# Performance work log

Measured on AMD Instinct MI355X. Metric: run time of the kernel, lower is better.

## Reference

```python
import jax, jax.numpy as jnp
import numpy as np

N = 100_000      # nodes
E = 3_200_000    # edges (avg degree 32)
D_IN = 128
D_H = 128
EPS = 1e-12      # F.normalize eps


def setup_inputs() -> dict:
    key = jax.random.key(0)
    k1, k2, k3 = jax.random.split(key, 3)
    X = jax.random.normal(k1, (N, D_IN), dtype=jnp.float32)
    edge_index = jax.random.randint(k2, (2, E), 0, N, dtype=jnp.int32)
    # GCNConv linear weight (stored as [in, out] for X @ W) and bias
    W = jax.random.normal(k3, (D_IN, D_H), dtype=jnp.float32) / np.sqrt(D_IN)
    b = jnp.zeros((D_H,), dtype=jnp.float32)
    # MessageNorm learnable scale, init 1.0
    scale = jnp.ones((1,), dtype=jnp.float32)
    return {"X": X, "edge_index": edge_index, "W": W, "b": b, "scale": scale}


def reference(X, edge_index, W, b, scale):
    n = X.shape[0]
    loop = jnp.arange(n, dtype=edge_index.dtype)
    src = jnp.concatenate([edge_index[0], loop])  # add self loops
    tgt = jnp.concatenate([edge_index[1], loop])
    # symmetric GCN normalization: D^{-1/2} (A+I) D^{-1/2}
    deg = jax.ops.segment_sum(jnp.ones_like(src, X.dtype), tgt, num_segments=n)
    dinv = jnp.where(deg > 0, jax.lax.rsqrt(deg), 0.0)
    norm = dinv[src] * dinv[tgt]  # [E+N]
    XW = X @ W  # [N, D_H]
    msg = jax.ops.segment_sum(norm[:, None] * XW[src], tgt, num_segments=n) + b
    # MessageNorm(learn_scale=True): l2-normalize msg, rescale by ||x||_2 * scale
    msg_n = msg / jnp.maximum(jnp.linalg.norm(msg, axis=-1, keepdims=True), EPS)
    x_norm = jnp.linalg.norm(X, axis=-1, keepdims=True)
    return jax.nn.gelu(msg_n * x_norm * scale, approximate=False)
```

## Files before the change

### kernel.cpp

```cpp
#include <hip/hip_runtime.h>
#include <math.h>

#define D 128
#define NB 391
#define BSH 8
#define BMASK 255
#define CAP 9216
#define EPB 4096
#define LDA 136

typedef unsigned short ushort_t;
typedef unsigned int uint_t;
typedef __attribute__((ext_vector_type(8))) short bfrag;
typedef __attribute__((ext_vector_type(4))) float ffrag;

__device__ inline ushort_t f2bf(float f) {
    uint_t u = __float_as_uint(f);
    uint_t r = (u + 0x7FFFu + ((u >> 16) & 1u)) >> 16;
    return (ushort_t)r;
}

__global__ __launch_bounds__(256) void k_bin(const int* __restrict__ src,
                                             const int* __restrict__ tgt, int e,
                                             int* __restrict__ bucket_cur,
                                             uint_t* __restrict__ binned,
                                             const float* __restrict__ W,
                                             ushort_t* __restrict__ Wt) {
    __shared__ uint_t sval[EPB];
    __shared__ ushort_t sbkt[EPB];
    __shared__ int lcnt[NB];
    __shared__ int lbeg[NB];
    __shared__ int gbase[NB];
    __shared__ int pscan[256];
    int tid = threadIdx.x;

    if (blockIdx.x < 16) {
        int nrow = blockIdx.x * 8 + (tid >> 5);
        int k0 = (tid & 31) * 4;
        ushort4 o;
        o.x = f2bf(W[(size_t)(k0 + 0) * D + nrow]);
        o.y = f2bf(W[(size_t)(k0 + 1) * D + nrow]);
        o.z = f2bf(W[(size_t)(k0 + 2) * D + nrow]);
        o.w = f2bf(W[(size_t)(k0 + 3) * D + nrow]);
        *(ushort4*)&Wt[(size_t)nrow * D + k0] = o;
    }

    int base = blockIdx.x * EPB;
    for (int i = tid; i < NB; i += 256) lcnt[i] = 0;
    __syncthreads();

    int myb[16];
    uint_t myval[16];
#pragma unroll
    for (int k = 0; k < 16; ++k) {
        int i = base + k * 256 + tid;
        if (i < e) {
            int t = tgt[i];
            int s = src[i];
            myb[k] = t >> BSH;
            myval[k] = ((uint_t)s << BSH) | (uint_t)(t & BMASK);
            atomicAdd(&lcnt[myb[k]], 1);
        } else {
            myb[k] = -1;
        }
    }
    __syncthreads();

    int c0 = (2 * tid < NB) ? lcnt[2 * tid] : 0;
    int c1 = (2 * tid + 1 < NB) ? lcnt[2 * tid + 1] : 0;
    int x = c0 + c1;
    pscan[tid] = x;
    __syncthreads();
    for (int off = 1; off < 256; off <<= 1) {
        int y = (tid >= off) ? pscan[tid - off] : 0;
        __syncthreads();
        x += y;
        pscan[tid] = x;
        __syncthreads();
    }
    int pb = x - (c0 + c1);
    if (2 * tid < NB) lbeg[2 * tid] = pb;
    if (2 * tid + 1 < NB) lbeg[2 * tid + 1] = pb + c0;
    __syncthreads();

    for (int i = tid; i < NB; i += 256) {
        int c = lcnt[i];
        gbase[i] = (c > 0) ? atomicAdd(&bucket_cur[i], c) : 0;
        lcnt[i] = lbeg[i];
    }
    __syncthreads();

#pragma unroll
    for (int k = 0; k < 16; ++k) {
        if (myb[k] >= 0) {
            int r = atomicAdd(&lcnt[myb[k]], 1);
            sval[r] = myval[k];
            sbkt[r] = (ushort_t)myb[k];
        }
    }
    __syncthreads();

    int nb = min(e - base, EPB);
    for (int i = tid; i < nb; i += 256) {
        int b = sbkt[i];
        int slot = gbase[b] + (i - lbeg[b]);
        if (slot < CAP) binned[(size_t)b * CAP + slot] = sval[i];
    }
}

__global__ __launch_bounds__(256) void k_mid(uint_t* __restrict__ binned,
                                             const int* __restrict__ bucket_cur,
                                             int* __restrict__ rowinfo,
                                             float* __restrict__ dinv,
                                             const float* __restrict__ X,
                                             const ushort_t* __restrict__ Wt,
                                             ushort_t* __restrict__ Y,
                                             float* __restrict__ xnorm, int n) {
    __shared__ __align__(16) char smem[52224];
    int tid = threadIdx.x;

    if (blockIdx.x < NB) {
        uint_t* sout = (uint_t*)smem;
        int* scnt  = (int*)(smem + CAP * 4);
        int* sincl = scnt + 256;
        int* sofs  = sincl + 256;
        int b = blockIdx.x;

        int nb = min(bucket_cur[b], CAP);
        uint_t* bin = binned + (size_t)b * CAP;

        scnt[tid] = 0;
        __syncthreads();
        for (int i = tid; i < nb; i += 256)
            atomicAdd(&scnt[bin[i] & BMASK], 1);
        __syncthreads();
        int x = scnt[tid];
        sincl[tid] = x;
        __syncthreads();
        for (int off = 1; off < 256; off <<= 1) {
            int y = (tid >= off) ? sincl[tid - off] : 0;
            __syncthreads();
            x += y;
            sincl[tid] = x;
            __syncthreads();
        }
        sofs[tid] = x - scnt[tid];
        int t = (b << BSH) + tid;
        if (t < n) {
            rowinfo[t] = ((x - scnt[tid]) << 16) | x;
            dinv[t] = rsqrtf((float)scnt[tid] + 1.0f);
        }
        __syncthreads();
        for (int i = tid; i < nb; i += 256) {
            uint_t w = bin[i];
            int r = atomicAdd(&sofs[w & BMASK], 1);
            sout[r] = w >> BSH;
        }
        __syncthreads();
        for (int i = tid; i < nb; i += 256)
            bin[i] = sout[i];
    } else {
        ushort_t* As = (ushort_t*)smem;
        ushort_t* Bs = (ushort_t*)(smem + 17408);
        int row0 = (blockIdx.x - NB) * 64;

        for (int i = tid; i < 128 * 16; i += 256) {
            int nr = i >> 4, c = (i & 15) << 3;
            *(uint4*)&Bs[nr * LDA + c] = *(const uint4*)&Wt[(size_t)nr * D + c];
        }

        const float4* X4 = (const float4*)X;
#pragma unroll
        for (int i2 = 0; i2 < 8; ++i2) {
            int item = i2 * 256 + tid;
            int r = item >> 5, c4 = item & 31;
            int gr = row0 + r;
            float4 vv = (gr < n) ? X4[(size_t)gr * 32 + c4] : make_float4(0.f, 0.f, 0.f, 0.f);
            ushort4 bv;
            bv.x = f2bf(vv.x); bv.y = f2bf(vv.y); bv.z = f2bf(vv.z); bv.w = f2bf(vv.w);
            *(ushort4*)&As[r * LDA + c4 * 4] = bv;
            float s = vv.x * vv.x + vv.y * vv.y + vv.z * vv.z + vv.w * vv.w;
            s += __shfl_xor(s, 1);
            s += __shfl_xor(s, 2);
            s += __shfl_xor(s, 4);
            s += __shfl_xor(s, 8);
            s += __shfl_xor(s, 16);
            if ((tid & 31) == 0 && gr < n) xnorm[gr] = sqrtf(s);
        }
        __syncthreads();

        int w = tid >> 6;
        int lane = tid & 63;
        int q = lane >> 4;
        int mi = lane & 15;

        bfrag xf[4];
#pragma unroll
        for (int kt = 0; kt < 4; ++kt)
            xf[kt] = *(const bfrag*)&As[(w * 16 + mi) * LDA + kt * 32 + q * 8];

        ffrag acc[8];
#pragma unroll
        for (int nt = 0; nt < 8; ++nt) acc[nt] = (ffrag){0.f, 0.f, 0.f, 0.f};

#pragma unroll
        for (int nt = 0; nt < 8; ++nt) {
#pragma unroll
            for (int kt = 0; kt < 4; ++kt) {
                bfrag wf = *(const bfrag*)&Bs[(nt * 16 + mi) * LDA + kt * 32 + q * 8];
                acc[nt] = __builtin_amdgcn_mfma_f32_16x16x32_bf16(wf, xf[kt], acc[nt], 0, 0, 0);
            }
        }

        __syncthreads();
#pragma unroll
        for (int nt = 0; nt < 8; ++nt) {
            ushort4 o;
            o.x = f2bf(acc[nt][0]);
            o.y = f2bf(acc[nt][1]);
            o.z = f2bf(acc[nt][2]);
            o.w = f2bf(acc[nt][3]);
            *(ushort4*)&As[(w * 16 + mi) * LDA + nt * 16 + q * 4] = o;
        }
        __syncthreads();

        int row = tid >> 2, seg = tid & 3;
        int grow = row0 + row;
        if (grow < n) {
#pragma unroll
            for (int k2 = 0; k2 < 4; ++k2) {
                uint4 vv = *(const uint4*)&As[row * LDA + seg * 32 + k2 * 8];
                *(uint4*)&Y[(size_t)grow * D + seg * 32 + k2 * 8] = vv;
            }
        }
    }
}

__global__ __launch_bounds__(256) void k_agg(const ushort_t* __restrict__ Y,
                                             const float* __restrict__ xnorm,
                                             const float* __restrict__ dinv,
                                             const int* __restrict__ rowinfo,
                                             const uint_t* __restrict__ binned,
                                             const float* __restrict__ bias,
                                             const float* __restrict__ scale,
                                             float* __restrict__ out, int n) {
    int t = (blockIdx.x * 256 + threadIdx.x) >> 6;
    int lane = threadIdx.x & 63;
    if (t >= n) return;

    const char* Yb = (const char*)Y;
    uint_t lo4 = (uint_t)lane * 4;
    float dt = dinv[t];

    uint_t p = *(const uint_t*)(Yb + (((uint_t)t << 8) + lo4));
    float a0 = dt * __uint_as_float(p << 16);
    float a1 = dt * __uint_as_float(p & 0xFFFF0000u);

    int ri = rowinfo[t];
    int slice = (t >> BSH) * CAP;
    int beg = slice + (ri >> 16);
    int end = slice + (ri & 0xFFFF);
    for (int base = beg; base < end; base += 64) {
        int m = min(end - base, 64);
        uint_t cv = binned[base + min(lane, m - 1)];
        int k = 0;
        for (; k + 16 <= m; k += 16) {
            uint_t qv[16];
            float dv[16];
#pragma unroll
            for (int j = 0; j < 16; ++j) {
                int s = __builtin_amdgcn_readlane((int)cv, k + j);
                dv[j] = dinv[s];
                qv[j] = *(const uint_t*)(Yb + ((size_t)(uint_t)s << 8) + lo4);
            }
#pragma unroll
            for (int j = 0; j < 16; ++j) {
                a0 = fmaf(dv[j], __uint_as_float(qv[j] << 16), a0);
                a1 = fmaf(dv[j], __uint_as_float(qv[j] & 0xFFFF0000u), a1);
            }
        }
        for (; k + 4 <= m; k += 4) {
            uint_t qv[4];
            float dv[4];
#pragma unroll
            for (int j = 0; j < 4; ++j) {
                int s = __builtin_amdgcn_readlane((int)cv, k + j);
                dv[j] = dinv[s];
                qv[j] = *(const uint_t*)(Yb + ((size_t)(uint_t)s << 8) + lo4);
            }
#pragma unroll
            for (int j = 0; j < 4; ++j) {
                a0 = fmaf(dv[j], __uint_as_float(qv[j] << 16), a0);
                a1 = fmaf(dv[j], __uint_as_float(qv[j] & 0xFFFF0000u), a1);
            }
        }
        for (; k < m; ++k) {
            int s = __builtin_amdgcn_readlane((int)cv, k);
            float dvs = dinv[s];
            uint_t q = *(const uint_t*)(Yb + ((size_t)(uint_t)s << 8) + lo4);
            a0 = fmaf(dvs, __uint_as_float(q << 16), a0);
            a1 = fmaf(dvs, __uint_as_float(q & 0xFFFF0000u), a1);
        }
    }

    float m0 = fmaf(dt, a0, bias[lane * 2]);
    float m1 = fmaf(dt, a1, bias[lane * 2 + 1]);

    float m2 = m0 * m0 + m1 * m1;
#pragma unroll
    for (int m = 32; m >= 1; m >>= 1) m2 += __shfl_xor(m2, m);

    float denom = fmaxf(sqrtf(m2), 1e-12f);
    float fac = xnorm[t] * scale[0] / denom;
    float g0 = m0 * fac;
    float g1 = m1 * fac;
    float2 o;
    o.x = 0.5f * g0 * (1.0f + erff(g0 * 0.70710678118654752440f));
    o.y = 0.5f * g1 * (1.0f + erff(g1 * 0.70710678118654752440f));
    *(float2*)&out[(size_t)t * D + lane * 2] = o;
}


extern "C" void kernel_launch(void* const* d_in, const int* in_sizes, int n_in,
                              void* d_out, int out_size, void* d_ws, size_t ws_size,
                              hipStream_t stream) {
    const float* X     = (const float*)d_in[0];
    const int*   ei    = (const int*)d_in[1];
    const float* W     = (const float*)d_in[2];
    const float* bias  = (const float*)d_in[3];
    const float* scale = (const float*)d_in[4];
    float* out = (float*)d_out;

    int n = in_sizes[0] / D;
    int e = in_sizes[1] / 2;
    const int* src = ei;
    const int* tgt = ei + e;

    char* ws = (char*)d_ws;
    ushort_t* Y = (ushort_t*)ws;   ws += (size_t)n * D * sizeof(ushort_t);
    uint_t* binned = (uint_t*)ws;  ws += (size_t)NB * CAP * sizeof(uint_t);
    float* dinv = (float*)ws;      ws += (size_t)n * sizeof(float);
    float* xnorm = (float*)ws;     ws += (size_t)n * sizeof(float);
    int* rowinfo = (int*)ws;       ws += (size_t)n * sizeof(int);
    int* bucket_cur = (int*)ws;    ws += NB * sizeof(int);
    ushort_t* Wt = (ushort_t*)ws;

    int ngemm = (n + 63) / 64;

    hipMemsetAsync(bucket_cur, 0, NB * sizeof(int), stream);
    k_bin<<<(e + EPB - 1) / EPB, 256, 0, stream>>>(src, tgt, e, bucket_cur, binned, W, Wt);
    k_mid<<<NB + ngemm, 256, 0, stream>>>(binned, bucket_cur, rowinfo, dinv, X, Wt, Y, xnorm, n);
    k_agg<<<(n + 3) / 4, 256, 0, stream>>>(Y, xnorm, dinv, rowinfo, binned, bias, scale, out, n);
}
```

Measured before the change: 288.4 us.

## Fuse bin, sort, GEMM and aggregation into one cooperative persistent kernel

Merges the memset and the three launches into a single cooperative kernel that uses grid.sync between phases, with a fallback to separate launches if the cooperative launch fails. The aim is to cut launch gaps and raise occupancy through smaller shared memory. Bucket size drops to 128 targets with half-sized chunks, so binning writes directly through per-thread ranks instead of staging in shared memory. The scans now use wave shuffles, and the GEMM reads W fragments from global memory instead of staging them in LDS. The costs are grid-wide barrier overhead, persistent-loop imbalance, and uncoalesced scattered binned writes.

```diff
diff --git a/kernel.cpp b/kernel.cpp
--- a/kernel.cpp
+++ b/kernel.cpp
@@ -1,13 +1,18 @@
 #include <hip/hip_runtime.h>
+#include <hip/hip_cooperative_groups.h>
 #include <math.h>
 
+namespace cg = cooperative_groups;
+
 #define D 128
-#define NB 391
-#define BSH 8
-#define BMASK 255
-#define CAP 9216
-#define EPB 4096
+#define BSH 7
+#define BMASK 127
+#define NT 128
+#define NB 782
+#define CAP 4608
+#define EPB 2048
 #define LDA 136
+#define SMEM_BYTES 20480
 
 typedef unsigned short ushort_t;
 typedef unsigned int uint_t;
@@ -20,22 +25,17 @@
     return (ushort_t)r;
 }
 
-__global__ __launch_bounds__(256) void k_bin(const int* __restrict__ src,
-                                             const int* __restrict__ tgt, int e,
-                                             int* __restrict__ bucket_cur,
-                                             uint_t* __restrict__ binned,
-                                             const float* __restrict__ W,
-                                             ushort_t* __restrict__ Wt) {
-    __shared__ uint_t sval[EPB];
-    __shared__ ushort_t sbkt[EPB];
-    __shared__ int lcnt[NB];
-    __shared__ int lbeg[NB];
-    __shared__ int gbase[NB];
-    __shared__ int pscan[256];
+__device__ void dev_bin(int v, int e, char* smem, const int* __restrict__ src,
+                        const int* __restrict__ tgt, int* __restrict__ bucket_cur,
+                        uint_t* __restrict__ binned, const float* __restrict__ W,
+                        ushort_t* __restrict__ Wt) {
+    int* lcnt = (int*)smem;
+    int* lbase = lcnt + NB;
     int tid = threadIdx.x;
-
-    if (blockIdx.x < 16) {
-        int nrow = blockIdx.x * 8 + (tid >> 5);
+    __syncthreads();
+
+    if (v < 16) {
+        int nrow = v * 8 + (tid >> 5);
         int k0 = (tid & 31) * 4;
         ushort4 o;
         o.x = f2bf(W[(size_t)(k0 + 0) * D + nrow]);
@@ -45,209 +45,173 @@
         *(ushort4*)&Wt[(size_t)nrow * D + k0] = o;
     }
 
-    int base = blockIdx.x * EPB;
+    int base = v * EPB;
     for (int i = tid; i < NB; i += 256) lcnt[i] = 0;
     __syncthreads();
 
-    int myb[16];
-    uint_t myval[16];
-#pragma unroll
-    for (int k = 0; k < 16; ++k) {
+    int myb[8], myrank[8];
+    uint_t myval[8];
+#pragma unroll
+    for (int k = 0; k < 8; ++k) {
         int i = base + k * 256 + tid;
         if (i < e) {
             int t = tgt[i];
             int s = src[i];
             myb[k] = t >> BSH;
             myval[k] = ((uint_t)s << BSH) | (uint_t)(t & BMASK);
-            atomicAdd(&lcnt[myb[k]], 1);
+            myrank[k] = atomicAdd(&lcnt[myb[k]], 1);
         } else {
             myb[k] = -1;
         }
     }
     __syncthreads();
-
-    int c0 = (2 * tid < NB) ? lcnt[2 * tid] : 0;
-    int c1 = (2 * tid + 1 < NB) ? lcnt[2 * tid + 1] : 0;
-    int x = c0 + c1;
-    pscan[tid] = x;
-    __syncthreads();
-    for (int off = 1; off < 256; off <<= 1) {
-        int y = (tid >= off) ? pscan[tid - off] : 0;
-        __syncthreads();
-        x += y;
-        pscan[tid] = x;
-        __syncthreads();
-    }
-    int pb = x - (c0 + c1);
-    if (2 * tid < NB) lbeg[2 * tid] = pb;
-    if (2 * tid + 1 < NB) lbeg[2 * tid + 1] = pb + c0;
-    __syncthreads();
-
     for (int i = tid; i < NB; i += 256) {
         int c = lcnt[i];
-        gbase[i] = (c > 0) ? atomicAdd(&bucket_cur[i], c) : 0;
-        lcnt[i] = lbeg[i];
-    }
-    __syncthreads();
-
-#pragma unroll
-    for (int k = 0; k < 16; ++k) {
+        lbase[i] = (c > 0) ? atomicAdd(&bucket_cur[i], c) : 0;
+    }
+    __syncthreads();
+#pragma unroll
+    for (int k = 0; k < 8; ++k) {
         if (myb[k] >= 0) {
-            int r = atomicAdd(&lcnt[myb[k]], 1);
-            sval[r] = myval[k];
-            sbkt[r] = (ushort_t)myb[k];
-        }
-    }
-    __syncthreads();
-
-    int nb = min(e - base, EPB);
-    for (int i = tid; i < nb; i += 256) {
-        int b = sbkt[i];
-        int slot = gbase[b] + (i - lbeg[b]);
-        if (slot < CAP) binned[(size_t)b * CAP + slot] = sval[i];
-    }
-}
-
-__global__ __launch_bounds__(256) void k_mid(uint_t* __restrict__ binned,
-                                             const int* __restrict__ bucket_cur,
-                                             int* __restrict__ rowinfo,
-                                             float* __restrict__ dinv,
-                                             const float* __restrict__ X,
-                                             const ushort_t* __restrict__ Wt,
-                                             ushort_t* __restrict__ Y,
-                                             float* __restrict__ xnorm, int n) {
-    __shared__ __align__(16) char smem[52224];
+            int slot = lbase[myb[k]] + myrank[k];
+            if (slot < CAP) binned[(size_t)myb[k] * CAP + slot] = myval[k];
+        }
+    }
+}
+
+__device__ void dev_sort(int b, int n, char* smem, uint_t* __restrict__ binned,
+                         const int* __restrict__ bucket_cur, int* __restrict__ rowinfo,
+                         float* __restrict__ dinv) {
+    uint_t* sout = (uint_t*)smem;
+    int* scnt = (int*)(smem + CAP * 4);
+    int* sbeg = scnt + NT;
+    int* sofs = sbeg + NT;
     int tid = threadIdx.x;
-
-    if (blockIdx.x < NB) {
-        uint_t* sout = (uint_t*)smem;
-        int* scnt  = (int*)(smem + CAP * 4);
-        int* sincl = scnt + 256;
-        int* sofs  = sincl + 256;
-        int b = blockIdx.x;
-
-        int nb = min(bucket_cur[b], CAP);
-        uint_t* bin = binned + (size_t)b * CAP;
-
-        scnt[tid] = 0;
-        __syncthreads();
-        for (int i = tid; i < nb; i += 256)
-            atomicAdd(&scnt[bin[i] & BMASK], 1);
-        __syncthreads();
-        int x = scnt[tid];
-        sincl[tid] = x;
-        __syncthreads();
-        for (int off = 1; off < 256; off <<= 1) {
-            int y = (tid >= off) ? sincl[tid - off] : 0;
-            __syncthreads();
-            x += y;
-            sincl[tid] = x;
-            __syncthreads();
-        }
-        sofs[tid] = x - scnt[tid];
+    int lane = tid & 63;
+    __syncthreads();
+
+    int nb = min(bucket_cur[b], CAP);
+    uint_t* bin = binned + (size_t)b * CAP;
+
+    if (tid < NT) scnt[tid] = 0;
+    __syncthreads();
+    for (int i = tid; i < nb; i += 256)
+        atomicAdd(&scnt[bin[i] & BMASK], 1);
+    __syncthreads();
+    if (tid < 64) {
+        int c0 = scnt[lane];
+        int c1 = scnt[lane + 64];
+        int x0 = c0, x1 = c1;
+#pragma unroll
+        for (int off = 1; off < 64; off <<= 1) {
+            int y0 = __shfl_up(x0, off);
+            int y1 = __shfl_up(x1, off);
+            if (lane >= off) { x0 += y0; x1 += y1; }
+        }
+        int tot0 = __shfl(x0, 63);
+        x1 += tot0;
+        sbeg[lane] = x0 - c0;      sofs[lane] = x0 - c0;
+        sbeg[lane + 64] = x1 - c1; sofs[lane + 64] = x1 - c1;
+    }
+    __syncthreads();
+    if (tid < NT) {
         int t = (b << BSH) + tid;
         if (t < n) {
-            rowinfo[t] = ((x - scnt[tid]) << 16) | x;
+            int beg = sbeg[tid];
+            rowinfo[t] = (beg << 16) | (beg + scnt[tid]);
             dinv[t] = rsqrtf((float)scnt[tid] + 1.0f);
         }
-        __syncthreads();
-        for (int i = tid; i < nb; i += 256) {
-            uint_t w = bin[i];
-            int r = atomicAdd(&sofs[w & BMASK], 1);
-            sout[r] = w >> BSH;
-        }
-        __syncthreads();
-        for (int i = tid; i < nb; i += 256)
-            bin[i] = sout[i];
-    } else {
-        ushort_t* As = (ushort_t*)smem;
-        ushort_t* Bs = (ushort_t*)(smem + 17408);
-        int row0 = (blockIdx.x - NB) * 64;
-
-        for (int i = tid; i < 128 * 16; i += 256) {
-            int nr = i >> 4, c = (i & 15) << 3;
-            *(uint4*)&Bs[nr * LDA + c] = *(const uint4*)&Wt[(size_t)nr * D + c];
-        }
-
-        const float4* X4 = (const float4*)X;
-#pragma unroll
-        for (int i2 = 0; i2 < 8; ++i2) {
-            int item = i2 * 256 + tid;
-            int r = item >> 5, c4 = item & 31;
-            int gr = row0 + r;
-            float4 vv = (gr < n) ? X4[(size_t)gr * 32 + c4] : make_float4(0.f, 0.f, 0.f, 0.f);
-            ushort4 bv;
-            bv.x = f2bf(vv.x); bv.y = f2bf(vv.y); bv.z = f2bf(vv.z); bv.w = f2bf(vv.w);
-            *(ushort4*)&As[r * LDA + c4 * 4] = bv;
-            float s = vv.x * vv.x + vv.y * vv.y + vv.z * vv.z + vv.w * vv.w;
-            s += __shfl_xor(s, 1);
-            s += __shfl_xor(s, 2);
-            s += __shfl_xor(s, 4);
-            s += __shfl_xor(s, 8);
-            s += __shfl_xor(s, 16);
-            if ((tid & 31) == 0 && gr < n) xnorm[gr] = sqrtf(s);
-        }
-        __syncthreads();
-
-        int w = tid >> 6;
-        int lane = tid & 63;
-        int q = lane >> 4;
-        int mi = lane & 15;
-
-        bfrag xf[4];
-#pragma unroll
-        for (int kt = 0; kt < 4; ++kt)
-            xf[kt] = *(const bfrag*)&As[(w * 16 + mi) * LDA + kt * 32 + q * 8];
-
-        ffrag acc[8];
-#pragma unroll
-        for (int nt = 0; nt < 8; ++nt) acc[nt] = (ffrag){0.f, 0.f, 0.f, 0.f};
-
-#pragma unroll
-        for (int nt = 0; nt < 8; ++nt) {
-#pragma unroll
-            for (int kt = 0; kt < 4; ++kt) {
-                bfrag wf = *(const bfrag*)&Bs[(nt * 16 + mi) * LDA + kt * 32 + q * 8];
-                acc[nt] = __builtin_amdgcn_mfma_f32_16x16x32_bf16(wf, xf[kt], acc[nt], 0, 0, 0);
-            }
-        }
-
-        __syncthreads();
-#pragma unroll
-        for (int nt = 0; nt < 8; ++nt) {
-            ushort4 o;
-            o.x = f2bf(acc[nt][0]);
-            o.y = f2bf(acc[nt][1]);
-            o.z = f2bf(acc[nt][2]);
-            o.w = f2bf(acc[nt][3]);
-            *(ushort4*)&As[(w * 16 + mi) * LDA + nt * 16 + q * 4] = o;
-        }
-        __syncthreads();
-
-        int row = tid >> 2, seg = tid & 3;
-        int grow = row0 + row;
-        if (grow < n) {
-#pragma unroll
-            for (int k2 = 0; k2 < 4; ++k2) {
-                uint4 vv = *(const uint4*)&As[row * LDA + seg * 32 + k2 * 8];
-                *(uint4*)&Y[(size_t)grow * D + seg * 32 + k2 * 8] = vv;
-            }
-        }
-    }
-}
-
-__global__ __launch_bounds__(256) void k_agg(const ushort_t* __restrict__ Y,
-                                             const float* __restrict__ xnorm,
-                                             const float* __restrict__ dinv,
-                                             const int* __restrict__ rowinfo,
-                                             const uint_t* __restrict__ binned,
-                                             const float* __restrict__ bias,
-                                             const float* __restrict__ scale,
-                                             float* __restrict__ out, int n) {
-    int t = (blockIdx.x * 256 + threadIdx.x) >> 6;
+    }
+    __syncthreads();
+    for (int i = tid; i < nb; i += 256) {
+        uint_t w = bin[i];
+        int r = atomicAdd(&sofs[w & BMASK], 1);
+        sout[r] = w >> BSH;
+    }
+    __syncthreads();
+    for (int i = tid; i < nb; i += 256)
+        bin[i] = sout[i];
+}
+
+__device__ void dev_gemm(int u, int n, char* smem, const float* __restrict__ X,
+                         const ushort_t* __restrict__ Wt, ushort_t* __restrict__ Y,
+                         float* __restrict__ xnorm) {
+    ushort_t* As = (ushort_t*)smem;
+    int tid = threadIdx.x;
+    int row0 = u * 64;
+    __syncthreads();
+
+    const float4* X4 = (const float4*)X;
+#pragma unroll
+    for (int i2 = 0; i2 < 8; ++i2) {
+        int item = i2 * 256 + tid;
+        int r = item >> 5, c4 = item & 31;
+        int gr = row0 + r;
+        float4 v = (gr < n) ? X4[(size_t)gr * 32 + c4] : make_float4(0.f, 0.f, 0.f, 0.f);
+        ushort4 bv;
+        bv.x = f2bf(v.x); bv.y = f2bf(v.y); bv.z = f2bf(v.z); bv.w = f2bf(v.w);
+        *(ushort4*)&As[r * LDA + c4 * 4] = bv;
+        float s = v.x * v.x + v.y * v.y + v.z * v.z + v.w * v.w;
+        s += __shfl_xor(s, 1);
+        s += __shfl_xor(s, 2);
+        s += __shfl_xor(s, 4);
+        s += __shfl_xor(s, 8);
+        s += __shfl_xor(s, 16);
+        if ((tid & 31) == 0 && gr < n) xnorm[gr] = sqrtf(s);
+    }
+    __syncthreads();
+
+    int w = tid >> 6;
+    int lane = tid & 63;
+    int q = lane >> 4;
+    int mi = lane & 15;
+
+    bfrag xf[4];
+#pragma unroll
+    for (int kt = 0; kt < 4; ++kt)
+        xf[kt] = *(const bfrag*)&As[(w * 16 + mi) * LDA + kt * 32 + q * 8];
+
+    ffrag acc[8];
+#pragma unroll
+    for (int nt = 0; nt < 8; ++nt) acc[nt] = (ffrag){0.f, 0.f, 0.f, 0.f};
+
+#pragma unroll
+    for (int nt = 0; nt < 8; ++nt) {
+#pragma unroll
+        for (int kt = 0; kt < 4; ++kt) {
+            bfrag wf = *(const bfrag*)&Wt[(size_t)(nt * 16 + mi) * D + kt * 32 + q * 8];
+            acc[nt] = __builtin_amdgcn_mfma_f32_16x16x32_bf16(wf, xf[kt], acc[nt], 0, 0, 0);
+        }
+    }
+
+    __syncthreads();
+#pragma unroll
+    for (int nt = 0; nt < 8; ++nt) {
+        ushort4 o;
+        o.x = f2bf(acc[nt][0]);
+        o.y = f2bf(acc[nt][1]);
+        o.z = f2bf(acc[nt][2]);
+        o.w = f2bf(acc[nt][3]);
+        *(ushort4*)&As[(w * 16 + mi) * LDA + nt * 16 + q * 4] = o;
+    }
+    __syncthreads();
+
+    int row = tid >> 2, seg = tid & 3;
+    int grow = row0 + row;
+    if (grow < n) {
+#pragma unroll
+        for (int k2 = 0; k2 < 4; ++k2) {
+            uint4 vv = *(const uint4*)&As[row * LDA + seg * 32 + k2 * 8];
+            *(uint4*)&Y[(size_t)grow * D + seg * 32 + k2 * 8] = vv;
+        }
+    }
+}
+
+__device__ void dev_agg(int t, const ushort_t* __restrict__ Y, const float* __restrict__ xnorm,
+                        const float* __restrict__ dinv, const int* __restrict__ rowinfo,
+                        const uint_t* __restrict__ binned, float b0, float b1, float sc,
+                        float* __restrict__ out) {
     int lane = threadIdx.x & 63;
-    if (t >= n) return;
-
     const char* Yb = (const char*)Y;
     uint_t lo4 = (uint_t)lane * 4;
     float dt = dinv[t];
@@ -303,21 +267,83 @@
         }
     }
 
-    float m0 = fmaf(dt, a0, bias[lane * 2]);
-    float m1 = fmaf(dt, a1, bias[lane * 2 + 1]);
-
+    float m0 = fmaf(dt, a0, b0);
+    float m1 = fmaf(dt, a1, b1);
     float m2 = m0 * m0 + m1 * m1;
 #pragma unroll
-    for (int m = 32; m >= 1; m >>= 1) m2 += __shfl_xor(m2, m);
-
+    for (int mm = 32; mm >= 1; mm >>= 1) m2 += __shfl_xor(m2, mm);
     float denom = fmaxf(sqrtf(m2), 1e-12f);
-    float fac = xnorm[t] * scale[0] / denom;
+    float fac = xnorm[t] * sc / denom;
     float g0 = m0 * fac;
     float g1 = m1 * fac;
     float2 o;
     o.x = 0.5f * g0 * (1.0f + erff(g0 * 0.70710678118654752440f));
     o.y = 0.5f * g1 * (1.0f + erff(g1 * 0.70710678118654752440f));
     *(float2*)&out[(size_t)t * D + lane * 2] = o;
+}
+
+__global__ __launch_bounds__(256, 6) void k_all(const int* src, const int* tgt, int e,
+                                                int* bucket_cur, uint_t* binned,
+                                                const float* W, ushort_t* Wt,
+                                                const float* X, ushort_t* Y, float* xnorm,
+                                                float* dinv, int* rowinfo,
+                                                const float* bias, const float* scale,
+                                                float* out, int n, int nchunk, int ngemm) {
+    cg::grid_group grid = cg::this_grid();
+    __shared__ __align__(16) char smem[SMEM_BYTES];
+    int nblk = gridDim.x;
+    int tid = threadIdx.x;
+
+    for (int i = blockIdx.x * 256 + tid; i < NB; i += nblk * 256) bucket_cur[i] = 0;
+    grid.sync();
+
+    for (int v = blockIdx.x; v < nchunk; v += nblk)
+        dev_bin(v, e, smem, src, tgt, bucket_cur, binned, W, Wt);
+    grid.sync();
+
+    int ntot = NB + ngemm;
+    for (int v = blockIdx.x; v < ntot; v += nblk) {
+        if (v < NB) dev_sort(v, n, smem, binned, bucket_cur, rowinfo, dinv);
+        else        dev_gemm(v - NB, n, smem, X, Wt, Y, xnorm);
+    }
+    grid.sync();
+
+    int lane = tid & 63;
+    float b0 = bias[lane * 2];
+    float b1 = bias[lane * 2 + 1];
+    float sc = scale[0];
+    int wid = blockIdx.x * 4 + (tid >> 6);
+    int nw = nblk * 4;
+    for (int t = wid; t < n; t += nw)
+        dev_agg(t, Y, xnorm, dinv, rowinfo, binned, b0, b1, sc, out);
+}
+
+__global__ __launch_bounds__(256) void k_bin_s(const int* src, const int* tgt, int e,
+                                               int* bucket_cur, uint_t* binned,
+                                               const float* W, ushort_t* Wt) {
+    __shared__ __align__(16) char smem[8192];
+    dev_bin(blockIdx.x, e, smem, src, tgt, bucket_cur, binned, W, Wt);
+}
+
+__global__ __launch_bounds__(256) void k_mid_s(uint_t* binned, const int* bucket_cur,
+                                               int* rowinfo, float* dinv, const float* X,
+                                               const ushort_t* Wt, ushort_t* Y,
+                                               float* xnorm, int n) {
+    __shared__ __align__(16) char smem[SMEM_BYTES];
+    int v = blockIdx.x;
+    if (v < NB) dev_sort(v, n, smem, binned, bucket_cur, rowinfo, dinv);
+    else        dev_gemm(v - NB, n, smem, X, Wt, Y, xnorm);
+}
+
+__global__ __launch_bounds__(256) void k_agg_s(const ushort_t* Y, const float* xnorm,
+                                               const float* dinv, const int* rowinfo,
+                                               const uint_t* binned, const float* bias,
+                                               const float* scale, float* out, int n) {
+    int t = (blockIdx.x * 256 + threadIdx.x) >> 6;
+    if (t >= n) return;
+    int lane = threadIdx.x & 63;
+    dev_agg(t, Y, xnorm, dinv, rowinfo, binned, bias[lane * 2], bias[lane * 2 + 1],
+            scale[0], out);
 }
 
 
@@ -345,10 +371,36 @@
     int* bucket_cur = (int*)ws;    ws += NB * sizeof(int);
     ushort_t* Wt = (ushort_t*)ws;
 
+    int nchunk = (e + EPB - 1) / EPB;
     int ngemm = (n + 63) / 64;
 
-    hipMemsetAsync(bucket_cur, 0, NB * sizeof(int), stream);
-    k_bin<<<(e + EPB - 1) / EPB, 256, 0, stream>>>(src, tgt, e, bucket_cur, binned, W, Wt);
-    k_mid<<<NB + ngemm, 256, 0, stream>>>(binned, bucket_cur, rowinfo, dinv, X, Wt, Y, xnorm, n);
-    k_agg<<<(n + 3) / 4, 256, 0, stream>>>(Y, xnorm, dinv, rowinfo, binned, bias, scale, out, n);
-}
+    static int coopGrid = -2;
+    if (coopGrid == -2) {
+        int occ = 0;
+        hipError_t oe = hipOccupancyMaxActiveBlocksPerMultiprocessor(&occ, k_all, 256, 0);
+        coopGrid = (oe == hipSuccess && occ >= 1) ? ((occ < 8 ? occ : 8) * 256) : -1;
+    }
+
+    bool done = false;
+    if (coopGrid > 0) {
+        const int* srcp = src; const int* tgtp = tgt;
+        int ev = e, nv = n, ncv = nchunk, ngv = ngemm;
+        int* bcur = bucket_cur; uint_t* binp = binned;
+        const float* Wp = W; ushort_t* Wtp = Wt;
+        const float* Xp = X; ushort_t* Yp = Y;
+        float* xnp = xnorm; float* dvp = dinv; int* rip = rowinfo;
+        const float* bp = bias; const float* scp = scale; float* op = out;
+        void* args[] = {&srcp, &tgtp, &ev, &bcur, &binp, &Wp, &Wtp, &Xp, &Yp,
+                        &xnp, &dvp, &rip, &bp, &scp, &op, &nv, &ncv, &ngv};
+        hipError_t err = hipLaunchCooperativeKernel((const void*)k_all, dim3(coopGrid),
+                                                    dim3(256), args, 0, stream);
+        if (err == hipSuccess) done = true;
+        else coopGrid = -1;
+    }
+    if (!done) {
+        hipMemsetAsync(bucket_cur, 0, NB * sizeof(int), stream);
+        k_bin_s<<<nchunk, 256, 0, stream>>>(src, tgt, e, bucket_cur, binned, W, Wt);
+        k_mid_s<<<NB + ngemm, 256, 0, stream>>>(binned, bucket_cur, rowinfo, dinv, X, Wt, Y, xnorm, n);
+        k_agg_s<<<(n + 3) / 4, 256, 0, stream>>>(Y, xnorm, dinv, rowinfo, binned, bias, scale, out, n);
+    }
+}
```

New measurement: 694.3 us. +140.7%, slower.
